# Kernel optimization log

Measured on AMD Instinct MI355X. Metric: run time of the kernel, lower is better.

The kernel has to match this reference:

```python
import jax, jax.numpy as jnp
import numpy as np

B, IN_DIM, HID = 4096, 1024, 1024


def _linear(x, W, b):
    # torch nn.Linear: y = x @ W.T + b, W is [out, in]
    return x @ W.T + b


def setup_inputs() -> dict:
    key = jax.random.key(0)
    ks = jax.random.split(key, 15)
    s_in = 1.0 / np.sqrt(IN_DIM + HID)
    s_x = 1.0 / np.sqrt(IN_DIM)
    s_h = 1.0 / np.sqrt(HID)
    return {
        "x": jax.random.normal(ks[0], (B, IN_DIM), jnp.float32),
        "h_prev": jax.random.normal(ks[1], (B, HID), jnp.float32),
        "c_prev": jax.random.normal(ks[2], (B, HID), jnp.float32),
        "Wi": jax.random.normal(ks[3], (HID, IN_DIM + HID), jnp.float32) * s_in,
        "bi": jax.random.normal(ks[4], (HID,), jnp.float32) * s_in,
        "Wf": jax.random.normal(ks[5], (HID, IN_DIM + HID), jnp.float32) * s_in,
        "bf": jax.random.normal(ks[6], (HID,), jnp.float32) * s_in,
        "Wo": jax.random.normal(ks[7], (HID, IN_DIM + HID), jnp.float32) * s_in,
        "bo": jax.random.normal(ks[8], (HID,), jnp.float32) * s_in,
        "Wxs": jax.random.normal(ks[9], (HID, IN_DIM), jnp.float32) * s_x,
        "bxs": jax.random.normal(ks[10], (HID,), jnp.float32) * s_x,
        "Wxg": jax.random.normal(ks[11], (HID, IN_DIM), jnp.float32) * s_x,
        "bxg": jax.random.normal(ks[12], (HID,), jnp.float32) * s_x,
        "Whg": jax.random.normal(ks[13], (HID, HID), jnp.float32) * s_h,
        "bhg": jax.random.normal(ks[14], (HID,), jnp.float32) * s_h,
    }


def reference(x, h_prev, c_prev, Wi, bi, Wf, bf, Wo, bo, Wxs, bxs, Wxg, bxg, Whg, bhg):
    # Fuse the three (in_dim+hid)->hid gate GEMMs into one concatenated GEMM.
    concat = jnp.concatenate([x, h_prev], axis=-1)          # [B, in_dim+hid]
    W_ifo = jnp.concatenate([Wi, Wf, Wo], axis=0)           # [3*hid, in_dim+hid]
    b_ifo = jnp.concatenate([bi, bf, bo], axis=0)           # [3*hid]
    gates = jax.nn.sigmoid(_linear(concat, W_ifo, b_ifo))   # [B, 3*hid]
    i_t, f_t, o_t = jnp.split(gates, 3, axis=-1)
    s_t = _linear(x, Wxs, bxs)
    cand_lin = _linear(x, Wxg, bxg) + _linear(h_prev, Whg, bhg)
    g_t = jnp.tanh(s_t * cand_lin)
    # refined=False branch
    c_t = f_t * c_prev + i_t * g_t
    h_t = o_t * jnp.tanh(c_t)
    return (h_t, c_t)
```

## Files before the change

kernel.cpp:

```cpp
#include <hip/hip_runtime.h>

typedef unsigned short u16;
typedef __attribute__((ext_vector_type(8))) __bf16 bf16x8;
typedef __attribute__((ext_vector_type(4))) float f32x4;
typedef __attribute__((ext_vector_type(4))) unsigned short u16x4;
typedef __attribute__((ext_vector_type(8))) unsigned short u16x8;

#define AS1 __attribute__((address_space(1)))
#define AS3 __attribute__((address_space(3)))

#define OB_X    0L
#define OB_H    4194304L
#define OB_WI   8388608L
#define OB_WF   10485760L
#define OB_WO   12582912L
#define OB_WXS  14680064L
#define OB_WXG  15728640L
#define OB_WHG  16777216L
#define BLOB_EL 17825792L

__device__ __forceinline__ u16 f2b(float f) {
    unsigned u = __float_as_uint(f);
    u += 0x7fffu + ((u >> 16) & 1u);
    return (u16)(u >> 16);
}

__global__ __launch_bounds__(256) void convert_all(
    const float* __restrict__ x, const float* __restrict__ h,
    const float* __restrict__ Wi, const float* __restrict__ Wf,
    const float* __restrict__ Wo, const float* __restrict__ Wxs,
    const float* __restrict__ Wxg, const float* __restrict__ Whg,
    u16* __restrict__ blob)
{
    long e = ((long)blockIdx.x * 256 + threadIdx.x) * 8;
    const float* src; long off;
    if      (e < OB_H)   { src = x;   off = e; }
    else if (e < OB_WI)  { src = h;   off = e - OB_H; }
    else if (e < OB_WF)  { src = Wi;  off = e - OB_WI; }
    else if (e < OB_WO)  { src = Wf;  off = e - OB_WF; }
    else if (e < OB_WXS) { src = Wo;  off = e - OB_WO; }
    else if (e < OB_WXG) { src = Wxs; off = e - OB_WXS; }
    else if (e < OB_WHG) { src = Wxg; off = e - OB_WXG; }
    else                 { src = Whg; off = e - OB_WHG; }
    f32x4 v0 = *(const f32x4*)(src + off);
    f32x4 v1 = *(const f32x4*)(src + off + 4);
    u16x8 o;
    o[0] = f2b(v0.x); o[1] = f2b(v0.y); o[2] = f2b(v0.z); o[3] = f2b(v0.w);
    o[4] = f2b(v1.x); o[5] = f2b(v1.y); o[6] = f2b(v1.z); o[7] = f2b(v1.w);
    *(u16x8*)(blob + e) = o;
}

__device__ __forceinline__ float sigf(float z) {
    return 1.f / (1.f + __expf(-z));
}

__device__ __forceinline__ void stage_tile(
    u16* As, u16* Bs, int k0,
    const u16* aLo, const u16* aHi,
    const u16* w0, const u16* w1, const u16* w2,
    const u16* w3lo, const u16* w3hi, const u16* w4,
    int t, int er, int gsw)
{
    const u16* aSrc = ((k0 < 1024) ? aLo : aHi) + (k0 & 1023) + gsw;
#pragma unroll
    for (int it = 0; it < 4; ++it) {
        __builtin_amdgcn_global_load_lds(
            (AS1 void*)(aSrc + (it * 64 + er) * 1024),
            (AS3 void*)(As + (it * 512 + t) * 8), 16, 0, 0);
    }
    __builtin_amdgcn_global_load_lds((AS1 void*)(w0 + k0 + er * 2048 + gsw),
        (AS3 void*)(Bs + t * 8), 16, 0, 0);
    __builtin_amdgcn_global_load_lds((AS1 void*)(w1 + k0 + er * 2048 + gsw),
        (AS3 void*)(Bs + 4096 + t * 8), 16, 0, 0);
    __builtin_amdgcn_global_load_lds((AS1 void*)(w2 + k0 + er * 2048 + gsw),
        (AS3 void*)(Bs + 8192 + t * 8), 16, 0, 0);
    const u16* w3 = (k0 < 1024) ? (w3lo + k0) : (w3hi + (k0 - 1024));
    __builtin_amdgcn_global_load_lds((AS1 void*)(w3 + er * 1024 + gsw),
        (AS3 void*)(Bs + 12288 + t * 8), 16, 0, 0);
    if (k0 < 1024)
        __builtin_amdgcn_global_load_lds((AS1 void*)(w4 + k0 + er * 1024 + gsw),
            (AS3 void*)(Bs + 16384 + t * 8), 16, 0, 0);
}

__device__ __forceinline__ void compute_tile(
    const u16* As, const u16* Bs, bool seg4,
    int wm, int wn, int fr, int fq, int r7,
    f32x4 (&acc)[5][4][2])
{
#pragma unroll
    for (int kk = 0; kk < 64; kk += 32) {
        const int sw = ((((kk >> 3) + fq) ^ r7) << 3);
        bf16x8 a[4];
#pragma unroll
        for (int mi = 0; mi < 4; ++mi)
            a[mi] = *(const bf16x8*)(As + (wm + mi * 16 + fr) * 64 + sw);
#pragma unroll
        for (int s = 0; s < 4; ++s) {
            bf16x8 b0 = *(const bf16x8*)(Bs + s * 4096 + (wn + fr) * 64 + sw);
            bf16x8 b1 = *(const bf16x8*)(Bs + s * 4096 + (wn + 16 + fr) * 64 + sw);
#pragma unroll
            for (int mi = 0; mi < 4; ++mi) {
                acc[s][mi][0] = __builtin_amdgcn_mfma_f32_16x16x32_bf16(
                    a[mi], b0, acc[s][mi][0], 0, 0, 0);
                acc[s][mi][1] = __builtin_amdgcn_mfma_f32_16x16x32_bf16(
                    a[mi], b1, acc[s][mi][1], 0, 0, 0);
            }
        }
        if (seg4) {
            bf16x8 b0 = *(const bf16x8*)(Bs + 16384 + (wn + fr) * 64 + sw);
            bf16x8 b1 = *(const bf16x8*)(Bs + 16384 + (wn + 16 + fr) * 64 + sw);
#pragma unroll
            for (int mi = 0; mi < 4; ++mi) {
                acc[4][mi][0] = __builtin_amdgcn_mfma_f32_16x16x32_bf16(
                    a[mi], b0, acc[4][mi][0], 0, 0, 0);
                acc[4][mi][1] = __builtin_amdgcn_mfma_f32_16x16x32_bf16(
                    a[mi], b1, acc[4][mi][1], 0, 0, 0);
            }
        }
    }
}

__global__ __launch_bounds__(512, 2) void srulstm_fused(
    const u16* __restrict__ blob,
    const float* __restrict__ c_prev,
    const float* __restrict__ bi, const float* __restrict__ bfv,
    const float* __restrict__ bo, const float* __restrict__ bxs,
    const float* __restrict__ bxg, const float* __restrict__ bhg,
    float* __restrict__ out)
{
    __shared__ __align__(16) u16 As[2][256 * 64];
    __shared__ __align__(16) u16 Bs[2][5 * 64 * 64];

    const u16* x = blob + OB_X;
    const u16* h = blob + OB_H;

    const int t = threadIdx.x;
    const int j0 = blockIdx.x * 64;
    const int m0 = blockIdx.y * 256;

    const u16* w0   = blob + OB_WI  + j0 * 2048;
    const u16* w1   = blob + OB_WF  + j0 * 2048;
    const u16* w2   = blob + OB_WO  + j0 * 2048;
    const u16* w3lo = blob + OB_WXG + j0 * 1024;
    const u16* w3hi = blob + OB_WHG + j0 * 1024;
    const u16* w4   = blob + OB_WXS + j0 * 1024;

    const u16* aLo = x + m0 * 1024;
    const u16* aHi = h + m0 * 1024;

    const int lane = t & 63;
    const int wave = t >> 6;
    const int wm = (wave >> 1) << 6;
    const int wn = (wave & 1) << 5;
    const int fr = lane & 15;
    const int fq = lane >> 4;
    const int r7 = fr & 7;

    const int er = t >> 3;
    const int gsw = (((t & 7) ^ (er & 7)) << 3);

    f32x4 acc[5][4][2] = {};

    stage_tile(As[0], Bs[0], 0, aLo, aHi, w0, w1, w2, w3lo, w3hi, w4, t, er, gsw);
    __syncthreads();

    for (int k0 = 0; k0 < 2048; k0 += 128) {
        stage_tile(As[1], Bs[1], k0 + 64,
                   aLo, aHi, w0, w1, w2, w3lo, w3hi, w4, t, er, gsw);
        compute_tile(As[0], Bs[0], k0 < 1024, wm, wn, fr, fq, r7, acc);
        __syncthreads();
        if (k0 + 128 < 2048)
            stage_tile(As[0], Bs[0], k0 + 128,
                       aLo, aHi, w0, w1, w2, w3lo, w3hi, w4, t, er, gsw);
        compute_tile(As[1], Bs[1], (k0 + 64) < 1024, wm, wn, fr, fq, r7, acc);
        __syncthreads();
    }

    const int orow = m0 + wm + (fq << 2);
    const int ocol = j0 + wn + fr;
#pragma unroll
    for (int ni = 0; ni < 2; ++ni) {
        const int col = ocol + ni * 16;
        const float bi_v = bi[col],  bf_v = bfv[col], bo_v = bo[col];
        const float bs_v = bxs[col], bg_v = bxg[col], bh_v = bhg[col];
#pragma unroll
        for (int mi = 0; mi < 4; ++mi) {
#pragma unroll
            for (int r = 0; r < 4; ++r) {
                const long idx = (long)(orow + mi * 16 + r) * 1024 + col;
                const float cp = c_prev[idx];
                const float i_t = sigf(acc[0][mi][ni][r] + bi_v);
                const float f_t = sigf(acc[1][mi][ni][r] + bf_v);
                const float o_t = sigf(acc[2][mi][ni][r] + bo_v);
                const float cand = acc[3][mi][ni][r] + bg_v + bh_v;
                const float s_t  = acc[4][mi][ni][r] + bs_v;
                const float g_t = tanhf(s_t * cand);
                const float c_t = f_t * cp + i_t * g_t;
                const float h_t = o_t * tanhf(c_t);
                out[idx] = h_t;
                out[4194304L + idx] = c_t;
            }
        }
    }
}

extern "C" void kernel_launch(void* const* d_in, const int* in_sizes, int n_in,
                              void* d_out, int out_size, void* d_ws, size_t ws_size,
                              hipStream_t stream)
{
    u16* blob = (u16*)d_ws;
    float* out = (float*)d_out;

    const long convBlocks = BLOB_EL / 8 / 256;

    convert_all<<<dim3(convBlocks), dim3(256), 0, stream>>>(
        (const float*)d_in[0], (const float*)d_in[1], (const float*)d_in[3],
        (const float*)d_in[5], (const float*)d_in[7], (const float*)d_in[9],
        (const float*)d_in[11], (const float*)d_in[13], blob);

    srulstm_fused<<<dim3(16, 16), dim3(512), 0, stream>>>(
        blob, (const float*)d_in[2], (const float*)d_in[4], (const float*)d_in[6],
        (const float*)d_in[8], (const float*)d_in[10], (const float*)d_in[12],
        (const float*)d_in[14], out);
}
```

Baseline: 247.3 us.

## Replace syncthreads double-buffering with vmcnt-gated barriers and split tile staging

The GEMM main loop now waits with explicit s_waitcnt vmcnt plus raw s_barrier instead of __syncthreads. Each step issues A and the first weight segment before the wait, then issues the other four weight segments between the two k-halves of compute, so global-to-LDS copies overlap the MFMA work more evenly. s_setprio is raised around the MFMA blocks to favour compute waves. To keep the vmcnt count fixed, the Wxs segment is now loaded on every step, including the second half of K where it is not used. That adds some redundant memory traffic.

```diff
diff --git a/kernel.cpp b/kernel.cpp
--- a/kernel.cpp
+++ b/kernel.cpp
@@ -3,7 +3,6 @@
 typedef unsigned short u16;
 typedef __attribute__((ext_vector_type(8))) __bf16 bf16x8;
 typedef __attribute__((ext_vector_type(4))) float f32x4;
-typedef __attribute__((ext_vector_type(4))) unsigned short u16x4;
 typedef __attribute__((ext_vector_type(8))) unsigned short u16x8;
 
 #define AS1 __attribute__((address_space(1)))
@@ -54,70 +53,90 @@
     return 1.f / (1.f + __expf(-z));
 }
 
-__device__ __forceinline__ void stage_tile(
-    u16* As, u16* Bs, int k0,
+__device__ __forceinline__ void stage_A(u16* An, int kS, const u16* aLo,
+                                        const u16* aHi, int t, int er, int gsw) {
+    const u16* aSrc = ((kS < 1024) ? aLo : aHi) + (kS & 1023) + gsw;
+#pragma unroll
+    for (int it = 0; it < 4; ++it)
+        __builtin_amdgcn_global_load_lds(
+            (AS1 void*)(aSrc + (it * 64 + er) * 1024),
+            (AS3 void*)(An + (it * 512 + t) * 8), 16, 0, 0);
+}
+
+__device__ __forceinline__ void stage_Bseg(u16* dst, const u16* src,
+                                           int t, int er, int gsw, int ld) {
+    __builtin_amdgcn_global_load_lds(
+        (AS1 void*)(src + er * ld + gsw),
+        (AS3 void*)(dst + t * 8), 16, 0, 0);
+}
+
+__device__ __forceinline__ void compute_half(
+    const u16* As, const u16* Bs, int kk, bool seg4,
+    int wm, int wn, int fr, int fq, int r7, f32x4 (&acc)[5][4][2])
+{
+    const int sw = ((((kk >> 3) + fq) ^ r7) << 3);
+    bf16x8 a[4];
+#pragma unroll
+    for (int mi = 0; mi < 4; ++mi)
+        a[mi] = *(const bf16x8*)(As + (wm + mi * 16 + fr) * 64 + sw);
+    __builtin_amdgcn_s_setprio(1);
+#pragma unroll
+    for (int s = 0; s < 4; ++s) {
+        bf16x8 b0 = *(const bf16x8*)(Bs + s * 4096 + (wn + fr) * 64 + sw);
+        bf16x8 b1 = *(const bf16x8*)(Bs + s * 4096 + (wn + 16 + fr) * 64 + sw);
+#pragma unroll
+        for (int mi = 0; mi < 4; ++mi) {
+            acc[s][mi][0] = __builtin_amdgcn_mfma_f32_16x16x32_bf16(
+                a[mi], b0, acc[s][mi][0], 0, 0, 0);
+            acc[s][mi][1] = __builtin_amdgcn_mfma_f32_16x16x32_bf16(
+                a[mi], b1, acc[s][mi][1], 0, 0, 0);
+        }
+    }
+    if (seg4) {
+        bf16x8 b0 = *(const bf16x8*)(Bs + 16384 + (wn + fr) * 64 + sw);
+        bf16x8 b1 = *(const bf16x8*)(Bs + 16384 + (wn + 16 + fr) * 64 + sw);
+#pragma unroll
+        for (int mi = 0; mi < 4; ++mi) {
+            acc[4][mi][0] = __builtin_amdgcn_mfma_f32_16x16x32_bf16(
+                a[mi], b0, acc[4][mi][0], 0, 0, 0);
+            acc[4][mi][1] = __builtin_amdgcn_mfma_f32_16x16x32_bf16(
+                a[mi], b1, acc[4][mi][1], 0, 0, 0);
+        }
+    }
+    __builtin_amdgcn_s_setprio(0);
+}
+
+template<bool STAGE, int VMC>
+__device__ __forceinline__ void tile_step(
+    const u16* Ac, const u16* Bc, u16* An, u16* Bn,
+    int k0, int kS,
     const u16* aLo, const u16* aHi,
     const u16* w0, const u16* w1, const u16* w2,
     const u16* w3lo, const u16* w3hi, const u16* w4,
-    int t, int er, int gsw)
-{
-    const u16* aSrc = ((k0 < 1024) ? aLo : aHi) + (k0 & 1023) + gsw;
-#pragma unroll
-    for (int it = 0; it < 4; ++it) {
-        __builtin_amdgcn_global_load_lds(
-            (AS1 void*)(aSrc + (it * 64 + er) * 1024),
-            (AS3 void*)(As + (it * 512 + t) * 8), 16, 0, 0);
-    }
-    __builtin_amdgcn_global_load_lds((AS1 void*)(w0 + k0 + er * 2048 + gsw),
-        (AS3 void*)(Bs + t * 8), 16, 0, 0);
-    __builtin_amdgcn_global_load_lds((AS1 void*)(w1 + k0 + er * 2048 + gsw),
-        (AS3 void*)(Bs + 4096 + t * 8), 16, 0, 0);
-    __builtin_amdgcn_global_load_lds((AS1 void*)(w2 + k0 + er * 2048 + gsw),
-        (AS3 void*)(Bs + 8192 + t * 8), 16, 0, 0);
-    const u16* w3 = (k0 < 1024) ? (w3lo + k0) : (w3hi + (k0 - 1024));
-    __builtin_amdgcn_global_load_lds((AS1 void*)(w3 + er * 1024 + gsw),
-        (AS3 void*)(Bs + 12288 + t * 8), 16, 0, 0);
-    if (k0 < 1024)
-        __builtin_amdgcn_global_load_lds((AS1 void*)(w4 + k0 + er * 1024 + gsw),
-            (AS3 void*)(Bs + 16384 + t * 8), 16, 0, 0);
-}
-
-__device__ __forceinline__ void compute_tile(
-    const u16* As, const u16* Bs, bool seg4,
+    int t, int er, int gsw,
     int wm, int wn, int fr, int fq, int r7,
     f32x4 (&acc)[5][4][2])
 {
-#pragma unroll
-    for (int kk = 0; kk < 64; kk += 32) {
-        const int sw = ((((kk >> 3) + fq) ^ r7) << 3);
-        bf16x8 a[4];
-#pragma unroll
-        for (int mi = 0; mi < 4; ++mi)
-            a[mi] = *(const bf16x8*)(As + (wm + mi * 16 + fr) * 64 + sw);
-#pragma unroll
-        for (int s = 0; s < 4; ++s) {
-            bf16x8 b0 = *(const bf16x8*)(Bs + s * 4096 + (wn + fr) * 64 + sw);
-            bf16x8 b1 = *(const bf16x8*)(Bs + s * 4096 + (wn + 16 + fr) * 64 + sw);
-#pragma unroll
-            for (int mi = 0; mi < 4; ++mi) {
-                acc[s][mi][0] = __builtin_amdgcn_mfma_f32_16x16x32_bf16(
-                    a[mi], b0, acc[s][mi][0], 0, 0, 0);
-                acc[s][mi][1] = __builtin_amdgcn_mfma_f32_16x16x32_bf16(
-                    a[mi], b1, acc[s][mi][1], 0, 0, 0);
-            }
-        }
-        if (seg4) {
-            bf16x8 b0 = *(const bf16x8*)(Bs + 16384 + (wn + fr) * 64 + sw);
-            bf16x8 b1 = *(const bf16x8*)(Bs + 16384 + (wn + 16 + fr) * 64 + sw);
-#pragma unroll
-            for (int mi = 0; mi < 4; ++mi) {
-                acc[4][mi][0] = __builtin_amdgcn_mfma_f32_16x16x32_bf16(
-                    a[mi], b0, acc[4][mi][0], 0, 0, 0);
-                acc[4][mi][1] = __builtin_amdgcn_mfma_f32_16x16x32_bf16(
-                    a[mi], b1, acc[4][mi][1], 0, 0, 0);
-            }
-        }
-    }
+    if (STAGE) {
+        stage_A(An, kS, aLo, aHi, t, er, gsw);
+        stage_Bseg(Bn, w0 + kS, t, er, gsw, 2048);
+    }
+    __builtin_amdgcn_sched_barrier(0);
+    asm volatile("s_waitcnt vmcnt(%0)" :: "n"(VMC) : "memory");
+    __builtin_amdgcn_s_barrier();
+    __builtin_amdgcn_sched_barrier(0);
+    compute_half(Ac, Bc, 0, k0 < 1024, wm, wn, fr, fq, r7, acc);
+    if (STAGE) {
+        stage_Bseg(Bn + 4096,  w1 + kS, t, er, gsw, 2048);
+        stage_Bseg(Bn + 8192,  w2 + kS, t, er, gsw, 2048);
+        const u16* w3 = (kS < 1024) ? (w3lo + kS) : (w3hi + (kS - 1024));
+        stage_Bseg(Bn + 12288, w3, t, er, gsw, 1024);
+        stage_Bseg(Bn + 16384, w4 + (kS & 1023), t, er, gsw, 1024);
+    }
+    compute_half(Ac, Bc, 32, k0 < 1024, wm, wn, fr, fq, r7, acc);
+    __builtin_amdgcn_sched_barrier(0);
+    __builtin_amdgcn_s_barrier();
+    __builtin_amdgcn_sched_barrier(0);
 }
 
 __global__ __launch_bounds__(512, 2) void srulstm_fused(
@@ -161,19 +180,25 @@
 
     f32x4 acc[5][4][2] = {};
 
-    stage_tile(As[0], Bs[0], 0, aLo, aHi, w0, w1, w2, w3lo, w3hi, w4, t, er, gsw);
-    __syncthreads();
+    stage_A(As[0], 0, aLo, aHi, t, er, gsw);
+    stage_Bseg(Bs[0],         w0, t, er, gsw, 2048);
+    stage_Bseg(Bs[0] + 4096,  w1, t, er, gsw, 2048);
+    stage_Bseg(Bs[0] + 8192,  w2, t, er, gsw, 2048);
+    stage_Bseg(Bs[0] + 12288, w3lo, t, er, gsw, 1024);
+    stage_Bseg(Bs[0] + 16384, w4, t, er, gsw, 1024);
 
     for (int k0 = 0; k0 < 2048; k0 += 128) {
-        stage_tile(As[1], Bs[1], k0 + 64,
-                   aLo, aHi, w0, w1, w2, w3lo, w3hi, w4, t, er, gsw);
-        compute_tile(As[0], Bs[0], k0 < 1024, wm, wn, fr, fq, r7, acc);
-        __syncthreads();
+        tile_step<true, 5>(As[0], Bs[0], As[1], Bs[1], k0, k0 + 64,
+                           aLo, aHi, w0, w1, w2, w3lo, w3hi, w4,
+                           t, er, gsw, wm, wn, fr, fq, r7, acc);
         if (k0 + 128 < 2048)
-            stage_tile(As[0], Bs[0], k0 + 128,
-                       aLo, aHi, w0, w1, w2, w3lo, w3hi, w4, t, er, gsw);
-        compute_tile(As[1], Bs[1], (k0 + 64) < 1024, wm, wn, fr, fq, r7, acc);
-        __syncthreads();
+            tile_step<true, 5>(As[1], Bs[1], As[0], Bs[0], k0 + 64, k0 + 128,
+                               aLo, aHi, w0, w1, w2, w3lo, w3hi, w4,
+                               t, er, gsw, wm, wn, fr, fq, r7, acc);
+        else
+            tile_step<false, 0>(As[1], Bs[1], As[0], Bs[0], k0 + 64, 0,
+                                aLo, aHi, w0, w1, w2, w3lo, w3hi, w4,
+                                t, er, gsw, wm, wn, fr, fq, r7, acc);
     }
 
     const int orow = m0 + wm + (fq << 2);
```

New measurement: 400.7 us. +62.1%, slower.
